# Kernel optimization log

Hardware: AMD Instinct MI355X
Metric: run time of the kernel (lower is better)

The kernel has to match this reference:

```python
import jax, jax.numpy as jnp
import numpy as np

NUM_HEADS = 8
EPS = 1e-6


def hamilton(a, b):
    # Quaternion (Hamilton) product on the last axis (size 4), broadcasting leading dims.
    aw, ax, ay, az = a[..., 0], a[..., 1], a[..., 2], a[..., 3]
    bw, bx, by, bz = b[..., 0], b[..., 1], b[..., 2], b[..., 3]
    return jnp.stack([
        aw * bw - ax * bx - ay * by - az * bz,
        aw * bx + ax * bw + ay * bz - az * by,
        aw * by - ax * bz + ay * bw + az * bx,
        aw * bz + ax * by - ay * bx + az * bw,
    ], axis=-1)


def setup_inputs() -> dict:
    key = jax.random.key(0)
    ks = jax.random.split(key, 7)
    B, L, E = 2, 384, 512
    s = 1.0 / np.sqrt(E)
    return {
        'x': jax.random.normal(ks[0], (B, L, E), dtype=jnp.float32),
        'Wq': jax.random.normal(ks[1], (E, E), dtype=jnp.float32) * s,
        'Wk': jax.random.normal(ks[2], (E, E), dtype=jnp.float32) * s,
        'Wv': jax.random.normal(ks[3], (E, E), dtype=jnp.float32) * s,
        'Wo': jax.random.normal(ks[4], (E, E), dtype=jnp.float32) * s,
        'dde_w': jax.random.normal(ks[5], (4, 4), dtype=jnp.float32) * 0.5,
        'dde_b': jnp.zeros((4,), dtype=jnp.float32),
    }


def reference(x, Wq, Wk, Wv, Wo, dde_w, dde_b):
    B, L, E = x.shape
    H = NUM_HEADS
    hd = E // H            # head_dim
    c = hd // 4            # quaternion atoms per head

    def proj_quat(W):
        # x @ W^T  -> split heads -> quaternion atoms: (B*H, L, c, 4)
        y = jnp.einsum('ble,fe->blf', x, W)
        y = y.reshape(B, L, H, hd).transpose(0, 2, 1, 3)  # (B,H,L,hd)
        return y.reshape(B * H, L, c, 4)

    q = proj_quat(Wq)
    k = proj_quat(Wk)
    v = proj_quat(Wv)

    # Broadcasted Hamilton product: (BH, L, L, c, 4)
    interference = hamilton(q[:, :, None, :, :], k[:, None, :, :, :])
    norm = jnp.linalg.norm(interference, axis=-1, keepdims=True) + EPS
    spinor = interference / norm

    # Discrete decision gate: mean over atoms -> (BH, L, L, 4) -> sigmoid(linear)
    gate_in = spinor.mean(axis=-2)
    gate = jax.nn.sigmoid(jnp.einsum('blmq,pq->blmp', gate_in, dde_w) + dde_b)
    spinor = spinor * gate[:, :, :, None, :]

    # Value aggregation: Hamilton product with v, summed over key positions j
    ctx = hamilton(spinor, v[:, None, :, :, :]).sum(axis=2)  # (BH, L, c, 4)

    ctx = ctx.reshape(B, H, L, hd).transpose(0, 2, 1, 3).reshape(B, L, E)
    return jnp.einsum('ble,fe->blf', ctx, Wo)
```

## Files before the change

kernel.cpp:

```cpp
#include <hip/hip_runtime.h>
#include <math.h>

#define L_SEQ 384
#define E_DIM 512
#define NHEAD 8
#define NBH   16
#define HD    64
#define LOG2E 1.44269504f

typedef __attribute__((ext_vector_type(8))) __bf16 bf16x8;
typedef __attribute__((ext_vector_type(8))) _Float16 f16x8;
typedef __attribute__((ext_vector_type(4))) float f32x4;

union u4h8 { uint4 u; f16x8 h; };

__device__ __forceinline__ float uniform_f(float v) {
  return __uint_as_float(__builtin_amdgcn_readfirstlane(__float_as_uint(v)));
}

__device__ __forceinline__ unsigned f2bf(float f) {
  unsigned u = __float_as_uint(f);
  return (u + 0x7FFFu + ((u >> 16) & 1u)) >> 16;
}

__device__ __forceinline__ unsigned ror16(unsigned x) { return (x >> 16) | (x << 16); }

__device__ __forceinline__ float dpp_xor1(float x) {
  return __int_as_float(__builtin_amdgcn_mov_dpp(__float_as_int(x), 0xB1, 0xF, 0xF, 0));
}
__device__ __forceinline__ float dpp_xor2(float x) {
  return __int_as_float(__builtin_amdgcn_mov_dpp(__float_as_int(x), 0x4E, 0xF, 0xF, 0));
}
template <int IMM>
__device__ __forceinline__ float swz_xor(float x) {
  return __int_as_float(__builtin_amdgcn_ds_swizzle(__float_as_int(x), IMM));
}

__device__ __forceinline__ size_t pidx(int row, int k, int Kd) {
  return ((((size_t)(row >> 4) * (Kd >> 5) + (k >> 5)) * 4 + ((k >> 3) & 3)) * 16
          + (row & 15)) * 8 + (k & 7);
}

__global__ __launch_bounds__(256) void to_bf16_all(
    const float* __restrict__ x, const float* __restrict__ Wq,
    const float* __restrict__ Wk, const float* __restrict__ Wv,
    const float* __restrict__ Wo, unsigned short* __restrict__ dst1,
    unsigned short* __restrict__ dst2, float* __restrict__ outz)
{
  int e0 = (blockIdx.x * 256 + threadIdx.x) * 4;
  if (e0 >= 1835008) return;
  if (e0 >= 1441792) {
    *(float4*)(outz + (e0 - 1441792)) = make_float4(0.f, 0.f, 0.f, 0.f);
    return;
  }
  const float* src; unsigned short* d; int s;
  if (e0 < 393216)       { src = x;  s = e0;           d = dst1; }
  else if (e0 < 655360)  { src = Wq; s = e0 - 393216;  d = dst1 + 393216; }
  else if (e0 < 917504)  { src = Wk; s = e0 - 655360;  d = dst1 + 655360; }
  else if (e0 < 1179648) { src = Wv; s = e0 - 917504;  d = dst1 + 917504; }
  else                   { src = Wo; s = e0 - 1179648; d = dst2; }
  float4 v = *(const float4*)(src + s);
  unsigned lo = f2bf(v.x) | (f2bf(v.y) << 16);
  unsigned hi = f2bf(v.z) | (f2bf(v.w) << 16);
  int row = s >> 9, k = s & 511;
  *(uint2*)(d + pidx(row, k, 512)) = make_uint2(lo, hi);
}

__global__ __launch_bounds__(256) void gemm_qkv(
    const __bf16* __restrict__ A, const __bf16* __restrict__ B0,
    const __bf16* __restrict__ B1, const __bf16* __restrict__ B2,
    float* __restrict__ C0, float* __restrict__ C1, float* __restrict__ C2,
    int M, int N, int K)
{
  const int z = blockIdx.z;
  const __bf16* Bm = (z == 0) ? B0 : (z == 1) ? B1 : B2;
  float* Cp = (z == 0) ? C0 : (z == 1) ? C1 : C2;

  const int tid = threadIdx.x;
  const int wave = tid >> 6, lane = tid & 63;
  const int m0 = blockIdx.y * 64 + wave * 16;
  const int n0 = blockIdx.x * 16;
  const int mr = lane & 15, quad = lane >> 4;
  const int KT = K >> 5;

  f32x4 acc = (f32x4){0.f, 0.f, 0.f, 0.f};

  const __bf16* ap = A + (size_t)(m0 >> 4) * KT * 512 + lane * 8;
  const __bf16* bp = Bm + (size_t)(n0 >> 4) * KT * 512 + lane * 8;

  #pragma unroll 4
  for (int ks = 0; ks < KT; ++ks) {
    bf16x8 a = *(const bf16x8*)(ap + (size_t)ks * 512);
    bf16x8 b = *(const bf16x8*)(bp + (size_t)ks * 512);
    acc = __builtin_amdgcn_mfma_f32_16x16x32_bf16(a, b, acc, 0, 0, 0);
  }

  _Float16* Hp = (_Float16*)Cp;
  int n = n0 + mr;
  #pragma unroll
  for (int r = 0; r < 4; ++r) {
    float val = acc[r];
    float s = val * val;
    s += dpp_xor1(s);
    s += dpp_xor2(s);
    float sc = (z == 2) ? 1.f : __builtin_amdgcn_rsqf(fmaxf(s, 1e-30f));
    int m = m0 + quad * 4 + r;
    int b = m / L_SEQ, l = m - b * L_SEQ;
    int row = (b * NHEAD + (n >> 6)) * L_SEQ + l;
    Hp[pidx(row, n & 63, 64)] = (_Float16)(val * sc);
  }
}

__global__ __launch_bounds__(256) void z_build(
    const _Float16* __restrict__ khh, const _Float16* __restrict__ vhh,
    _Float16* __restrict__ Z0)
{
  const int tid = threadIdx.x;
  const int l = blockIdx.x * 64 + (tid & 63);
  const int a = blockIdx.y * 4 + (tid >> 6);
  const int bh = blockIdx.z;

  size_t off = pidx(bh * L_SEQ + l, a * 4, 64);
  union { uint2 u; _Float16 h[4]; } kk, vv;
  kk.u = *(const uint2*)(khh + off);
  vv.u = *(const uint2*)(vhh + off);

  float kb[4] = {(float)kk.h[0], (float)kk.h[1], (float)kk.h[2], (float)kk.h[3]};
  float ve[4] = {(float)vv.h[0], (float)vv.h[1], (float)vv.h[2], (float)vv.h[3]};
  _Float16* zp = Z0 + (size_t)bh * (256 * 384);
  #pragma unroll
  for (int b = 0; b < 4; ++b)
    #pragma unroll
    for (int e = 0; e < 4; ++e)
      zp[pidx(a * 16 + b * 4 + e, l, 384)] = (_Float16)(kb[b] * ve[e]);
}

__global__ __launch_bounds__(256) void gate_pv(
    const _Float16* __restrict__ qhh, const _Float16* __restrict__ khh,
    const _Float16* __restrict__ Z0, const float* __restrict__ dde_w,
    const float* __restrict__ dde_b, const __bf16* __restrict__ Wob,
    float* __restrict__ out)
{
  __shared__ _Float16 gbuf[2][4096];
  __shared__ float qs[16][65];
  __shared__ __bf16 ctx_lds[16][72];

  const int tid = threadIdx.x, w = tid >> 6, lane = tid & 63;
  const int mr = lane & 15, quad = lane >> 4;
  const int bh = blockIdx.y, ib = blockIdx.x;
  const int i0 = ib * 16;

  {
    int il = tid >> 4, k4 = (tid & 15) * 4;
    union { uint2 u; _Float16 h[4]; } cv;
    cv.u = *(const uint2*)(qhh + pidx(bh * L_SEQ + i0 + il, k4, 64));
    qs[il][k4 + 0] = (float)cv.h[0]; qs[il][k4 + 1] = (float)cv.h[1];
    qs[il][k4 + 2] = (float)cv.h[2]; qs[il][k4 + 3] = (float)cv.h[3];
  }

  float wn[16], bn[4];
  #pragma unroll
  for (int t = 0; t < 16; ++t) wn[t] = uniform_f(dde_w[t]) * (-LOG2E * 0.0625f);
  #pragma unroll
  for (int c = 0; c < 4; ++c) bn[c] = uniform_f(dde_b[c]) * (-LOG2E);

  u4h8 fr[4][2];
  {
    const _Float16* ap = qhh + ((size_t)(bh * 24 + ib)) * 2 * 512 + lane * 8;
    #pragma unroll
    for (int ks = 0; ks < 2; ++ks) {
      uint4 qa = *(const uint4*)(ap + ks * 512);
      unsigned s0 = ror16(qa.x), s1 = ror16(qa.y), s2 = ror16(qa.z), s3 = ror16(qa.w);
      fr[0][ks].u = make_uint4(qa.x ^ 0x80000000u, qa.y ^ 0x80008000u,
                               qa.z ^ 0x80000000u, qa.w ^ 0x80008000u);
      fr[1][ks].u = make_uint4(s0, s1 ^ 0x00008000u, s2, s3 ^ 0x00008000u);
      fr[2][ks].u = make_uint4(qa.y, qa.x ^ 0x80000000u, qa.w, qa.z ^ 0x80000000u);
      fr[3][ks].u = make_uint4(s1 ^ 0x80000000u, s0, s3 ^ 0x80000000u, s2);
    }
  }

  const int bq = mr >> 2, e = mr & 3;
  unsigned msk[4];
  #pragma unroll
  for (int c = 0; c < 4; ++c)
    msk[c] = ((((0x284Eu >> (c * 4 + bq)) ^ (0xC6A0u >> (c * 4 + e))) & 1u) << 31);

  f32x4 acc[4][4];
  #pragma unroll
  for (int c = 0; c < 4; ++c)
    #pragma unroll
    for (int nt = 0; nt < 4; ++nt) acc[c][nt] = (f32x4){0.f, 0.f, 0.f, 0.f};

  const int jl = w * 16 + mr;
  const int gw = (jl >> 3) * 128 + (jl & 7) + quad * 32;

  #pragma unroll 2
  for (int ch = 0; ch < 6; ++ch) {
    u4h8 zb[2][4];
    #pragma unroll
    for (int ks2 = 0; ks2 < 2; ++ks2)
      #pragma unroll
      for (int nt = 0; nt < 4; ++nt)
        zb[ks2][nt].h = *(const f16x8*)(Z0 + (size_t)bh * (256 * 384)
                         + (((size_t)(w * 4 + nt) * 12 + ch * 2 + ks2) * 512) + lane * 8);

    const _Float16* bp = khh + ((size_t)(bh * 24 + ch * 4 + w)) * 2 * 512 + lane * 8;
    u4h8 kb[2];
    kb[0].h = *(const f16x8*)(bp);
    kb[1].h = *(const f16x8*)(bp + 512);
    f32x4 accS[4];
    #pragma unroll
    for (int c = 0; c < 4; ++c) {
      accS[c] = (f32x4){0.f, 0.f, 0.f, 0.f};
      accS[c] = __builtin_amdgcn_mfma_f32_16x16x32_f16(fr[c][0].h, kb[0].h, accS[c], 0, 0, 0);
      accS[c] = __builtin_amdgcn_mfma_f32_16x16x32_f16(fr[c][1].h, kb[1].h, accS[c], 0, 0, 0);
    }

    #pragma unroll
    for (int r = 0; r < 4; ++r) {
      float S0 = accS[0][r], S1 = accS[1][r], S2 = accS[2][r], S3 = accS[3][r];
      #pragma unroll
      for (int c = 0; c < 4; ++c) {
        float n = bn[c] + wn[c*4+0]*S0 + wn[c*4+1]*S1 + wn[c*4+2]*S2 + wn[c*4+3]*S3;
        float g = __builtin_amdgcn_rcpf(1.f + __builtin_amdgcn_exp2f(n));
        gbuf[ch & 1][c * 1024 + gw + r * 8] = (_Float16)g;
      }
    }
    __syncthreads();

    #pragma unroll
    for (int ks2 = 0; ks2 < 2; ++ks2) {
      #pragma unroll
      for (int c = 0; c < 4; ++c) {
        f16x8 aa = *(const f16x8*)&gbuf[ch & 1][c * 1024 + ks2 * 512 + lane * 8];
        #pragma unroll
        for (int nt = 0; nt < 4; ++nt)
          acc[c][nt] = __builtin_amdgcn_mfma_f32_16x16x32_f16(aa, zb[ks2][nt].h, acc[c][nt], 0, 0, 0);
      }
    }
  }

  #pragma unroll
  for (int nt = 0; nt < 4; ++nt) {
    #pragma unroll
    for (int r = 0; r < 4; ++r) {
      int il = quad * 4 + r;
      float pb[4];
      #pragma unroll
      for (int c = 0; c < 4; ++c) {
        float sq = __uint_as_float(
            __float_as_uint(qs[il][w * 16 + nt * 4 + (bq ^ c)]) ^ msk[c]);
        float v = sq * acc[c][nt][r];
        v += swz_xor<0x101F>(v);
        v += swz_xor<0x201F>(v);
        pb[c] = v;
      }
      float q0 = pb[0] + dpp_xor1(pb[1]);
      float q1 = pb[1] + dpp_xor1(pb[0]);
      float q2 = pb[2] + dpp_xor1(pb[3]);
      float q3 = pb[3] + dpp_xor1(pb[2]);
      float r0 = q0 + dpp_xor2(q2);
      float r1 = q1 + dpp_xor2(q3);
      float r2 = q2 + dpp_xor2(q0);
      float r3 = q3 + dpp_xor2(q1);
      if (mr == 0) {
        ctx_lds[il][w * 16 + nt * 4 + 0] = (__bf16)r0;
        ctx_lds[il][w * 16 + nt * 4 + 1] = (__bf16)r1;
        ctx_lds[il][w * 16 + nt * 4 + 2] = (__bf16)r2;
        ctx_lds[il][w * 16 + nt * 4 + 3] = (__bf16)r3;
      }
    }
  }
  __syncthreads();

  const int bb_ = bh >> 3, hh = bh & 7;
  const int m_base = bb_ * L_SEQ + i0;
  bf16x8 af[2];
  #pragma unroll
  for (int ks2 = 0; ks2 < 2; ++ks2)
    af[ks2] = *(const bf16x8*)&ctx_lds[mr][ks2 * 32 + quad * 8];
  #pragma unroll
  for (int nt2 = 0; nt2 < 8; ++nt2) {
    const int ntile = w * 8 + nt2;
    f32x4 accO = (f32x4){0.f, 0.f, 0.f, 0.f};
    #pragma unroll
    for (int ks2 = 0; ks2 < 2; ++ks2) {
      bf16x8 b = *(const bf16x8*)(Wob + ((size_t)ntile * 16 + hh * 2 + ks2) * 512 + lane * 8);
      accO = __builtin_amdgcn_mfma_f32_16x16x32_bf16(af[ks2], b, accO, 0, 0, 0);
    }
    const int n = ntile * 16 + mr;
    #pragma unroll
    for (int r = 0; r < 4; ++r) {
      int m = m_base + quad * 4 + r;
      __hip_atomic_fetch_add(&out[(size_t)m * E_DIM + n], accO[r],
                             __ATOMIC_RELAXED, __HIP_MEMORY_SCOPE_AGENT);
    }
  }
}

extern "C" void kernel_launch(void* const* d_in, const int* in_sizes, int n_in,
                              void* d_out, int out_size, void* d_ws, size_t ws_size,
                              hipStream_t stream)
{
  const float* x     = (const float*)d_in[0];
  const float* Wq    = (const float*)d_in[1];
  const float* Wk    = (const float*)d_in[2];
  const float* Wv    = (const float*)d_in[3];
  const float* Wo    = (const float*)d_in[4];
  const float* dde_w = (const float*)d_in[5];
  const float* dde_b = (const float*)d_in[6];
  float* out = (float*)d_out;

  char* ws = (char*)d_ws;
  unsigned short* Wob  = (unsigned short*)(ws + 0);
  _Float16* qhh = (_Float16*)(ws + 524288);
  _Float16* khh = (_Float16*)(ws + 1310720);
  _Float16* Z0h = (_Float16*)(ws + 2097152);
  _Float16* vhh = (_Float16*)(ws + 5242880);
  unsigned short* xb  = (unsigned short*)(ws + 6029312);
  unsigned short* Wqb = (unsigned short*)(ws + 6815744);
  unsigned short* Wkb = (unsigned short*)(ws + 7340032);
  unsigned short* Wvb = (unsigned short*)(ws + 7864320);

  to_bf16_all<<<1792, 256, 0, stream>>>(x, Wq, Wk, Wv, Wo, xb, Wob, out);

  gemm_qkv<<<dim3(32, 12, 3), 256, 0, stream>>>(
      (const __bf16*)xb, (const __bf16*)Wqb, (const __bf16*)Wkb, (const __bf16*)Wvb,
      (float*)qhh, (float*)khh, (float*)vhh, 2 * L_SEQ, E_DIM, E_DIM);

  z_build<<<dim3(6, 4, 16), 256, 0, stream>>>(khh, vhh, Z0h);

  gate_pv<<<dim3(24, 16), 256, 0, stream>>>(
      qhh, khh, Z0h, dde_w, dde_b, (const __bf16*)Wob, out);
}
```

Before: 103.0 us.

## Fuse K/V projection with Z outer-product build and prefetch K tiles

Merges the z_build kernel into the QKV GEMM. The K and V projections are computed together in one block, and the k⊗v products are written to Z0 straight from registers using DPP quad broadcasts. This removes one kernel launch and the vhh round trip through global memory. It also double-buffers the K tile loads in gate_pv so the next chunk's loads overlap the current chunk's gate computation. The cost is fewer GEMM blocks (z=2 instead of 3), with the K/V blocks doing twice the work, plus a fully unrolled loop that raises register pressure.

```diff
diff --git a/kernel.cpp b/kernel.cpp
--- a/kernel.cpp
+++ b/kernel.cpp
@@ -30,6 +30,10 @@
 }
 __device__ __forceinline__ float dpp_xor2(float x) {
   return __int_as_float(__builtin_amdgcn_mov_dpp(__float_as_int(x), 0x4E, 0xF, 0xF, 0));
+}
+template <int PAT>
+__device__ __forceinline__ float quad_bcast(float x) {
+  return __int_as_float(__builtin_amdgcn_mov_dpp(__float_as_int(x), PAT, 0xF, 0xF, 0));
 }
 template <int IMM>
 __device__ __forceinline__ float swz_xor(float x) {
@@ -69,70 +73,77 @@
 __global__ __launch_bounds__(256) void gemm_qkv(
     const __bf16* __restrict__ A, const __bf16* __restrict__ B0,
     const __bf16* __restrict__ B1, const __bf16* __restrict__ B2,
-    float* __restrict__ C0, float* __restrict__ C1, float* __restrict__ C2,
-    int M, int N, int K)
+    _Float16* __restrict__ qhh, _Float16* __restrict__ khh,
+    _Float16* __restrict__ Z0)
 {
   const int z = blockIdx.z;
-  const __bf16* Bm = (z == 0) ? B0 : (z == 1) ? B1 : B2;
-  float* Cp = (z == 0) ? C0 : (z == 1) ? C1 : C2;
-
   const int tid = threadIdx.x;
   const int wave = tid >> 6, lane = tid & 63;
   const int m0 = blockIdx.y * 64 + wave * 16;
   const int n0 = blockIdx.x * 16;
   const int mr = lane & 15, quad = lane >> 4;
-  const int KT = K >> 5;
-
-  f32x4 acc = (f32x4){0.f, 0.f, 0.f, 0.f};
+  const int KT = 16;
 
   const __bf16* ap = A + (size_t)(m0 >> 4) * KT * 512 + lane * 8;
-  const __bf16* bp = Bm + (size_t)(n0 >> 4) * KT * 512 + lane * 8;
-
-  #pragma unroll 4
-  for (int ks = 0; ks < KT; ++ks) {
-    bf16x8 a = *(const bf16x8*)(ap + (size_t)ks * 512);
-    bf16x8 b = *(const bf16x8*)(bp + (size_t)ks * 512);
-    acc = __builtin_amdgcn_mfma_f32_16x16x32_bf16(a, b, acc, 0, 0, 0);
-  }
-
-  _Float16* Hp = (_Float16*)Cp;
-  int n = n0 + mr;
-  #pragma unroll
-  for (int r = 0; r < 4; ++r) {
-    float val = acc[r];
-    float s = val * val;
-    s += dpp_xor1(s);
-    s += dpp_xor2(s);
-    float sc = (z == 2) ? 1.f : __builtin_amdgcn_rsqf(fmaxf(s, 1e-30f));
-    int m = m0 + quad * 4 + r;
-    int b = m / L_SEQ, l = m - b * L_SEQ;
-    int row = (b * NHEAD + (n >> 6)) * L_SEQ + l;
-    Hp[pidx(row, n & 63, 64)] = (_Float16)(val * sc);
-  }
-}
-
-__global__ __launch_bounds__(256) void z_build(
-    const _Float16* __restrict__ khh, const _Float16* __restrict__ vhh,
-    _Float16* __restrict__ Z0)
-{
-  const int tid = threadIdx.x;
-  const int l = blockIdx.x * 64 + (tid & 63);
-  const int a = blockIdx.y * 4 + (tid >> 6);
-  const int bh = blockIdx.z;
-
-  size_t off = pidx(bh * L_SEQ + l, a * 4, 64);
-  union { uint2 u; _Float16 h[4]; } kk, vv;
-  kk.u = *(const uint2*)(khh + off);
-  vv.u = *(const uint2*)(vhh + off);
-
-  float kb[4] = {(float)kk.h[0], (float)kk.h[1], (float)kk.h[2], (float)kk.h[3]};
-  float ve[4] = {(float)vv.h[0], (float)vv.h[1], (float)vv.h[2], (float)vv.h[3]};
-  _Float16* zp = Z0 + (size_t)bh * (256 * 384);
-  #pragma unroll
-  for (int b = 0; b < 4; ++b)
-    #pragma unroll
-    for (int e = 0; e < 4; ++e)
-      zp[pidx(a * 16 + b * 4 + e, l, 384)] = (_Float16)(kb[b] * ve[e]);
+  const int n = n0 + mr;
+
+  if (z == 0) {
+    const __bf16* bp = B0 + (size_t)(n0 >> 4) * KT * 512 + lane * 8;
+    f32x4 acc = (f32x4){0.f, 0.f, 0.f, 0.f};
+    #pragma unroll 4
+    for (int ks = 0; ks < KT; ++ks) {
+      bf16x8 a = *(const bf16x8*)(ap + (size_t)ks * 512);
+      bf16x8 b = *(const bf16x8*)(bp + (size_t)ks * 512);
+      acc = __builtin_amdgcn_mfma_f32_16x16x32_bf16(a, b, acc, 0, 0, 0);
+    }
+    #pragma unroll
+    for (int r = 0; r < 4; ++r) {
+      float val = acc[r];
+      float s = val * val;
+      s += dpp_xor1(s);
+      s += dpp_xor2(s);
+      float sc = __builtin_amdgcn_rsqf(fmaxf(s, 1e-30f));
+      int m = m0 + quad * 4 + r;
+      int b = m / L_SEQ, l = m - b * L_SEQ;
+      int row = (b * NHEAD + (n >> 6)) * L_SEQ + l;
+      qhh[pidx(row, n & 63, 64)] = (_Float16)(val * sc);
+    }
+  } else {
+    const __bf16* bpk = B1 + (size_t)(n0 >> 4) * KT * 512 + lane * 8;
+    const __bf16* bpv = B2 + (size_t)(n0 >> 4) * KT * 512 + lane * 8;
+    f32x4 accK = (f32x4){0.f, 0.f, 0.f, 0.f};
+    f32x4 accV = (f32x4){0.f, 0.f, 0.f, 0.f};
+    #pragma unroll 4
+    for (int ks = 0; ks < KT; ++ks) {
+      bf16x8 a = *(const bf16x8*)(ap + (size_t)ks * 512);
+      bf16x8 bk = *(const bf16x8*)(bpk + (size_t)ks * 512);
+      bf16x8 bv = *(const bf16x8*)(bpv + (size_t)ks * 512);
+      accK = __builtin_amdgcn_mfma_f32_16x16x32_bf16(a, bk, accK, 0, 0, 0);
+      accV = __builtin_amdgcn_mfma_f32_16x16x32_bf16(a, bv, accV, 0, 0, 0);
+    }
+    const int a_atom = (n & 63) >> 2, comp = n & 3;
+    #pragma unroll
+    for (int r = 0; r < 4; ++r) {
+      float vk = accK[r], vv = accV[r];
+      float s = vk * vk;
+      s += dpp_xor1(s);
+      s += dpp_xor2(s);
+      float kn = vk * __builtin_amdgcn_rsqf(fmaxf(s, 1e-30f));
+      int m = m0 + quad * 4 + r;
+      int b = m / L_SEQ, l = m - b * L_SEQ;
+      int bh = b * NHEAD + (n >> 6);
+      int row = bh * L_SEQ + l;
+      khh[pidx(row, n & 63, 64)] = (_Float16)kn;
+      float v0 = quad_bcast<0x00>(vv), v1 = quad_bcast<0x55>(vv);
+      float v2 = quad_bcast<0xAA>(vv), v3 = quad_bcast<0xFF>(vv);
+      _Float16* zp = Z0 + (size_t)bh * (256 * 384);
+      int colb = a_atom * 16 + comp * 4;
+      zp[pidx(colb + 0, l, 384)] = (_Float16)(kn * v0);
+      zp[pidx(colb + 1, l, 384)] = (_Float16)(kn * v1);
+      zp[pidx(colb + 2, l, 384)] = (_Float16)(kn * v2);
+      zp[pidx(colb + 3, l, 384)] = (_Float16)(kn * v3);
+    }
+  }
 }
 
 __global__ __launch_bounds__(256) void gate_pv(
@@ -194,8 +205,16 @@
   const int jl = w * 16 + mr;
   const int gw = (jl >> 3) * 128 + (jl & 7) + quad * 32;
 
-  #pragma unroll 2
+  u4h8 kbp[2][2];
+  {
+    const _Float16* bp = khh + ((size_t)(bh * 24 + w)) * 2 * 512 + lane * 8;
+    kbp[0][0].h = *(const f16x8*)(bp);
+    kbp[0][1].h = *(const f16x8*)(bp + 512);
+  }
+
+  #pragma unroll
   for (int ch = 0; ch < 6; ++ch) {
+    const int cur = ch & 1, nxt = cur ^ 1;
     u4h8 zb[2][4];
     #pragma unroll
     for (int ks2 = 0; ks2 < 2; ++ks2)
@@ -204,16 +223,18 @@
         zb[ks2][nt].h = *(const f16x8*)(Z0 + (size_t)bh * (256 * 384)
                          + (((size_t)(w * 4 + nt) * 12 + ch * 2 + ks2) * 512) + lane * 8);
 
-    const _Float16* bp = khh + ((size_t)(bh * 24 + ch * 4 + w)) * 2 * 512 + lane * 8;
-    u4h8 kb[2];
-    kb[0].h = *(const f16x8*)(bp);
-    kb[1].h = *(const f16x8*)(bp + 512);
     f32x4 accS[4];
     #pragma unroll
     for (int c = 0; c < 4; ++c) {
       accS[c] = (f32x4){0.f, 0.f, 0.f, 0.f};
-      accS[c] = __builtin_amdgcn_mfma_f32_16x16x32_f16(fr[c][0].h, kb[0].h, accS[c], 0, 0, 0);
-      accS[c] = __builtin_amdgcn_mfma_f32_16x16x32_f16(fr[c][1].h, kb[1].h, accS[c], 0, 0, 0);
+      accS[c] = __builtin_amdgcn_mfma_f32_16x16x32_f16(fr[c][0].h, kbp[cur][0].h, accS[c], 0, 0, 0);
+      accS[c] = __builtin_amdgcn_mfma_f32_16x16x32_f16(fr[c][1].h, kbp[cur][1].h, accS[c], 0, 0, 0);
+    }
+
+    if (ch < 5) {
+      const _Float16* bp = khh + ((size_t)(bh * 24 + (ch + 1) * 4 + w)) * 2 * 512 + lane * 8;
+      kbp[nxt][0].h = *(const f16x8*)(bp);
+      kbp[nxt][1].h = *(const f16x8*)(bp + 512);
     }
 
     #pragma unroll
@@ -223,7 +244,7 @@
       for (int c = 0; c < 4; ++c) {
         float n = bn[c] + wn[c*4+0]*S0 + wn[c*4+1]*S1 + wn[c*4+2]*S2 + wn[c*4+3]*S3;
         float g = __builtin_amdgcn_rcpf(1.f + __builtin_amdgcn_exp2f(n));
-        gbuf[ch & 1][c * 1024 + gw + r * 8] = (_Float16)g;
+        gbuf[cur][c * 1024 + gw + r * 8] = (_Float16)g;
       }
     }
     __syncthreads();
@@ -232,7 +253,7 @@
     for (int ks2 = 0; ks2 < 2; ++ks2) {
       #pragma unroll
       for (int c = 0; c < 4; ++c) {
-        f16x8 aa = *(const f16x8*)&gbuf[ch & 1][c * 1024 + ks2 * 512 + lane * 8];
+        f16x8 aa = *(const f16x8*)&gbuf[cur][c * 1024 + ks2 * 512 + lane * 8];
         #pragma unroll
         for (int nt = 0; nt < 4; ++nt)
           acc[c][nt] = __builtin_amdgcn_mfma_f32_16x16x32_f16(aa, zb[ks2][nt].h, acc[c][nt], 0, 0, 0);
@@ -316,7 +337,6 @@
   _Float16* qhh = (_Float16*)(ws + 524288);
   _Float16* khh = (_Float16*)(ws + 1310720);
   _Float16* Z0h = (_Float16*)(ws + 2097152);
-  _Float16* vhh = (_Float16*)(ws + 5242880);
   unsigned short* xb  = (unsigned short*)(ws + 6029312);
   unsigned short* Wqb = (unsigned short*)(ws + 6815744);
   unsigned short* Wkb = (unsigned short*)(ws + 7340032);
@@ -324,11 +344,9 @@
 
   to_bf16_all<<<1792, 256, 0, stream>>>(x, Wq, Wk, Wv, Wo, xb, Wob, out);
 
-  gemm_qkv<<<dim3(32, 12, 3), 256, 0, stream>>>(
+  gemm_qkv<<<dim3(32, 12, 2), 256, 0, stream>>>(
       (const __bf16*)xb, (const __bf16*)Wqb, (const __bf16*)Wkb, (const __bf16*)Wvb,
-      (float*)qhh, (float*)khh, (float*)vhh, 2 * L_SEQ, E_DIM, E_DIM);
-
-  z_build<<<dim3(6, 4, 16), 256, 0, stream>>>(khh, vhh, Z0h);
+      qhh, khh, Z0h);
 
   gate_pv<<<dim3(24, 16), 256, 0, stream>>>(
       qhh, khh, Z0h, dde_w, dde_b, (const __bf16*)Wob, out);
```

After: 101.3 us (median of 2 runs). About the same (-1.6%).
